# Performance work log

Measured on AMD Instinct MI355X. Metric: run time of the kernel, lower is better.

## Reference

```python
import jax, jax.numpy as jnp
import numpy as np

T, B, L, S = 2048, 64, 32, 256
NEG = -1e30  # effective -inf, safe under logaddexp


def setup_inputs() -> dict:
    key = jax.random.key(0)
    k1, k2, k3 = jax.random.split(key, 3)
    inputs = jax.random.normal(k1, (T, B, L), dtype=jnp.float32)
    targets = jax.random.randint(k2, (B, S), 0, L)
    input_lengths = jnp.full((B,), T, dtype=jnp.int32)
    target_lengths = jnp.full((B,), S, dtype=jnp.int32)
    # learned transition matrix (param of ASGLoss); small random for a non-trivial test
    transition = 0.1 * jax.random.normal(k3, (L, L), dtype=jnp.float32)
    return {"transition": transition, "inputs": inputs, "targets": targets,
            "input_lengths": input_lengths, "target_lengths": target_lengths}


def _fcc_scores(transition, inputs, input_lengths):
    # Fully-connected forward: alpha_t[i] = emit_t[i] + logsumexp_j(alpha_{t-1}[j] + trans[i,j])
    alpha0 = inputs[0]  # [B, L]

    def step(alpha, emit):
        new = emit + jax.nn.logsumexp(alpha[:, None, :] + transition[None, :, :], axis=2)
        return new, new

    _, rest = jax.lax.scan(step, alpha0, inputs[1:])
    alphas = jnp.concatenate([alpha0[None], rest], axis=0)  # [T, B, L]
    b = jnp.arange(inputs.shape[1])
    # causal DP: alpha at t = len-1 is exactly the score for that length
    return jax.nn.logsumexp(alphas[input_lengths - 1, b], axis=-1)  # [B]


def _fac_scores(transition, inputs, targets, input_lengths, target_lengths):
    # Force-aligned forward over target positions s:
    # alpha_t[s] = emit_t[tgt_s] + logaddexp(alpha_{t-1}[s] + trans[tgt_s,tgt_s],
    #                                        alpha_{t-1}[s-1] + trans[tgt_s,tgt_{s-1}])
    Tn, Bn, _ = inputs.shape
    Sn = targets.shape[1]
    # gathered emissions for target labels: [T, B, S]
    emit = jnp.take_along_axis(inputs, jnp.broadcast_to(targets[None], (Tn, Bn, Sn)), axis=2)
    self_tr = transition[targets, targets]                       # [B, S] stay score
    prev = jnp.concatenate([targets[:, :1], targets[:, :-1]], 1)
    move_tr = transition[targets, prev]                          # [B, S] move score (s=0 unused)

    alpha0 = jnp.where((jnp.arange(Sn) == 0)[None, :], emit[0], NEG)  # only s=0 at t=0

    def step(alpha, e):
        stay = alpha + self_tr
        moved = jnp.concatenate(
            [jnp.full_like(alpha[:, :1], NEG), alpha[:, :-1] + move_tr[:, 1:]], axis=1)
        new = e + jnp.logaddexp(stay, moved)
        return new, new

    _, rest = jax.lax.scan(step, alpha0, emit[1:])
    alphas = jnp.concatenate([alpha0[None], rest], axis=0)  # [T, B, S]
    b = jnp.arange(Bn)
    return alphas[input_lengths - 1, b, target_lengths - 1]  # [B]


def reference(transition, inputs, targets, input_lengths, target_lengths):
    # original clamps targets to input length; S <= T here so it's a no-op
    fcc = _fcc_scores(transition, inputs, input_lengths)
    fac = _fac_scores(transition, inputs, targets, input_lengths, target_lengths)
    result = fcc - fac  # [B]
    return result.mean()  # reduction='mean'
```

## Files before the change

### kernel.cpp

```cpp
#include <hip/hip_runtime.h>
#include <math.h>

static constexpr int TB = 64;
static constexpr int LL = 32;
static constexpr int SS = 256;
static constexpr int STRIDE_T = TB * LL;

static constexpr int NCH = 16;
static constexpr int NI  = NCH - 2;
static constexpr int NSCAN = 2 + 2 * NI;

static constexpr int OF_FCC  = 0;
static constexpr int OF_FACF = 992;
static constexpr int OF_FACB = 1312;
static constexpr int WSB     = 1632;
static constexpr int OF_DIFF = TB * WSB;

#define LN2F 0.69314718055994530942f
#define NEGF (-1e30f)
#define SBAR() __builtin_amdgcn_sched_barrier(0)

#define BARX() { asm volatile("s_waitcnt lgkmcnt(0)" ::: "memory"); \
                 __builtin_amdgcn_s_barrier(); \
                 asm volatile("" ::: "memory"); }

template<int CTL>
__device__ __forceinline__ float dpp_f(float x, float oldv) {
  return __int_as_float(__builtin_amdgcn_update_dpp(
      __float_as_int(oldv), __float_as_int(x), CTL, 0xF, 0xF, false));
}
template<int M>
__device__ __forceinline__ int rot_i(int x) {
  return __builtin_amdgcn_update_dpp(0, x, 0x120 + M, 0xF, 0xF, false);
}

typedef unsigned uint2v __attribute__((ext_vector_type(2)));
__device__ __forceinline__ float xsum16(float x) {
  uint2v r = __builtin_amdgcn_permlane16_swap(__float_as_uint(x), __float_as_uint(x), false, false);
  return __uint_as_float(r.x) + __uint_as_float(r.y);
}
__device__ __forceinline__ float xsum32(float x) {
  uint2v r = __builtin_amdgcn_permlane32_swap(__float_as_uint(x), __float_as_uint(x), false, false);
  return __uint_as_float(r.x) + __uint_as_float(r.y);
}
__device__ __forceinline__ float bperm(int addr, float src) {
  return __int_as_float(__builtin_amdgcn_ds_bpermute(addr, __float_as_int(src)));
}

template<int M>
struct Calib {
  __device__ static __forceinline__ void run(const float* trans, int lam, int i, float* Ec) {
    Ec[M] = __expf(trans[i * LL + rot_i<M>(lam)]);
    Calib<M + 1>::run(trans, lam, i, Ec);
  }
};
template<> struct Calib<16> {
  __device__ static __forceinline__ void run(const float*, int, int, float*) {}
};
template<int M>
struct CalibT {
  __device__ static __forceinline__ void run(const float* trans, int lam, int i, float* Ec) {
    Ec[M] = __expf(trans[rot_i<M>(lam) * LL + i]);
    CalibT<M + 1>::run(trans, lam, i, Ec);
  }
};
template<> struct CalibT<16> {
  __device__ static __forceinline__ void run(const float*, int, int, float*) {}
};

#define ROT_MUL(DST, SRC, COEF, ROT) \
  asm("v_mul_f32_dpp %0, %1, %2 row_ror:" #ROT " row_mask:0xf bank_mask:0xf" \
      : "=v"(DST) : "v"(SRC), "v"(COEF))
#define ROT_FMAC(ACC, SRC, COEF, ROT) \
  asm("v_fmac_f32_dpp %0, %1, %2 row_ror:" #ROT " row_mask:0xf bank_mask:0xf" \
      : "+v"(ACC) : "v"(SRC), "v"(COEF))

#define STEP16(EC) { \
  float a0 = EC[0] * A, a1, a2, a3, a4, a5, a6, a7; \
  ROT_MUL(a1, A, EC[1], 1); ROT_MUL(a2, A, EC[2], 2); ROT_MUL(a3, A, EC[3], 3); \
  ROT_MUL(a4, A, EC[4], 4); ROT_MUL(a5, A, EC[5], 5); ROT_MUL(a6, A, EC[6], 6); \
  ROT_MUL(a7, A, EC[7], 7); \
  ROT_FMAC(a0, A, EC[8], 8);   ROT_FMAC(a1, A, EC[9], 9); \
  ROT_FMAC(a2, A, EC[10], 10); ROT_FMAC(a3, A, EC[11], 11); \
  ROT_FMAC(a4, A, EC[12], 12); ROT_FMAC(a5, A, EC[13], 13); \
  ROT_FMAC(a6, A, EC[14], 14); ROT_FMAC(a7, A, EC[15], 15); \
  part = ((a0 + a1) + (a2 + a3)) + ((a4 + a5) + (a6 + a7)); }


#define FCC_RENORM() { \
  unsigned uu = (unsigned)__builtin_amdgcn_readfirstlane((int)__float_as_uint(A)); \
  int ex = (int)((uu >> 23) & 255) - 127; \
  A = ldexpf(A, -ex); Kt += ex; }

#define LDBLK(R, TBASE) { \
  _Pragma("unroll") for (int k = 0; k < 4; ++k) { \
    int tt = (TBASE) + 2 * k + rowoff; tt = tt > lenm1 ? lenm1 : tt; \
    R[k] = gpl[(size_t)tt * STRIDE_T]; } \
  SBAR(); }
#define LDBLKD(R, TBASE) { \
  _Pragma("unroll") for (int k = 0; k < 4; ++k) { \
    int tt = (TBASE) + 2 * k + rowoff; \
    tt = tt < 0 ? 0 : (tt > lenm1 ? lenm1 : tt); \
    R[k] = gpl[(size_t)tt * STRIDE_T]; } \
  SBAR(); }

#define FCC_BLOCK8(R) { \
  float eb[8]; \
  _Pragma("unroll") for (int k = 0; k < 4; ++k) { \
    float e_ = __expf(R[k]); \
    eb[2 * k]     = bperm(adE, e_); \
    eb[2 * k + 1] = bperm(adO, e_); } \
  { float part; STEP16(Ec1); A = eb[0] * xsum16(part); } \
  { float part; STEP16(Ec2); A = eb[1] * xsum32(part); } \
  { float part; STEP16(Ec1); A = eb[2] * xsum16(part); } \
  { float part; STEP16(Ec2); A = eb[3] * xsum32(part); } \
  { float part; STEP16(Ec1); A = eb[4] * xsum16(part); } \
  { float part; STEP16(Ec2); A = eb[5] * xsum32(part); } \
  { float part; STEP16(Ec1); A = eb[6] * xsum16(part); } \
  { float part; STEP16(Ec2); A = eb[7] * xsum32(part); } \
  FCC_RENORM(); }

#define FCC_BWDBLK8(R) { \
  float eb[8]; \
  _Pragma("unroll") for (int k = 0; k < 4; ++k) { \
    float e_ = __expf(R[k]); \
    eb[2 * k]     = bperm(adE, e_); \
    eb[2 * k + 1] = bperm(adO, e_); } \
  { A *= eb[7]; float part; STEP16(E1T); A = xsum16(part); } \
  { A *= eb[6]; float part; STEP16(E2T); A = xsum32(part); } \
  { A *= eb[5]; float part; STEP16(E1T); A = xsum16(part); } \
  { A *= eb[4]; float part; STEP16(E2T); A = xsum32(part); } \
  { A *= eb[3]; float part; STEP16(E1T); A = xsum16(part); } \
  { A *= eb[2]; float part; STEP16(E2T); A = xsum32(part); } \
  { A *= eb[1]; float part; STEP16(E1T); A = xsum16(part); } \
  { A *= eb[0]; float part; STEP16(E2T); A = xsum32(part); } \
  FCC_RENORM(); }


#define FAC_BOUNDARY_S() { \
  float maxA = fmaxf(fmaxf(A0, A1), fmaxf(A2, A3)); \
  if (maxA > 0.f) { \
    int ex = (int)((__float_as_uint(maxA) >> 23) & 255) - 127; \
    A0 = ldexpf(A0, -ex); A1 = ldexpf(A1, -ex); \
    A2 = ldexpf(A2, -ex); A3 = ldexpf(A3, -ex); \
    m += (float)ex; \
  } \
  float mp = dpp_f<0x138>(m, NEGF); m = (m == NEGF) ? mp : m; \
  mp = dpp_f<0x138>(m, NEGF);       m = (m == NEGF) ? mp : m; \
  mp = dpp_f<0x138>(m, NEGF); \
  float dlt = fminf(mp - m, 50.0f); \
  Sin = exp2f(dlt); }

#define FACB_BOUNDARY_S() { \
  float maxA = fmaxf(fmaxf(A0, A1), fmaxf(A2, A3)); \
  if (maxA > 0.f) { \
    int ex = (int)((__float_as_uint(maxA) >> 23) & 255) - 127; \
    A0 = ldexpf(A0, -ex); A1 = ldexpf(A1, -ex); \
    A2 = ldexpf(A2, -ex); A3 = ldexpf(A3, -ex); \
    m += (float)ex; \
  } \
  float mp = dpp_f<0x130>(m, NEGF); m = (m == NEGF) ? mp : m; \
  mp = dpp_f<0x130>(m, NEGF);       m = (m == NEGF) ? mp : m; \
  mp = dpp_f<0x130>(m, NEGF); \
  float dlt = fminf(mp - m, 50.0f); \
  Sb = exp2f(dlt); }

#define FRDGRP(PB, BASE) { \
  _Pragma("unroll") for (int r = 0; r < 8; ++r) { \
    e0[r] = sE[PB][(BASE) + r][tg[0]]; \
    e1[r] = sE[PB][(BASE) + r][tg[1]]; \
    e2[r] = sE[PB][(BASE) + r][tg[2]]; \
    e3[r] = sE[PB][(BASE) + r][tg[3]]; } \
  SBAR(); }

#define FSTEPN(R) { \
  float c0 = e0[R] * ST[0], c1 = e1[R] * ST[1]; \
  float c2 = e2[R] * ST[2], c3 = e3[R] * ST[3]; \
  float v0 = e0[R] * CM[0], v1 = e1[R] * CM[1]; \
  float v2 = e2[R] * CM[2], v3 = e3[R] * CM[3]; \
  float ap = dpp_f<0x138>(A3, 0.f);  \
  float n0 = fmaf(v0 * Sin, ap, c0 * A0); \
  float n1 = fmaf(v1, A0, c1 * A1); \
  float n2 = fmaf(v2, A1, c2 * A2); \
  float n3 = fmaf(v3, A2, c3 * A3); \
  A0 = n0; A1 = n1; A2 = n2; A3 = n3; }

#define FBSTEPN(R) { \
  float c0 = e0[R] * ST[0], c1 = e1[R] * ST[1]; \
  float c2 = e2[R] * ST[2], c3 = e3[R] * ST[3]; \
  float w0 = e1[R] * CM[0], w1 = e2[R] * CM[1], w2 = e3[R] * CM[2]; \
  float en3 = dpp_f<0x130>(e0[R], 0.f);  \
  float w3 = en3 * CM[3]; \
  float an = dpp_f<0x130>(A0, 0.f); \
  float n0 = fmaf(w0, A1, c0 * A0); \
  float n1 = fmaf(w1, A2, c1 * A1); \
  float n2 = fmaf(w2, A3, c2 * A2); \
  float n3 = fmaf(w3 * Sb, an, c3 * A3); \
  A0 = n0; A1 = n1; A2 = n2; A3 = n3; }

#define FACF_CON32N(PB) { \
  float e0[8], e1[8], e2[8], e3[8]; \
  FRDGRP(PB, 0); \
  _Pragma("unroll") for (int r = 0; r < 8; ++r) FSTEPN(r); \
  FAC_BOUNDARY_S(); \
  FRDGRP(PB, 8); \
  _Pragma("unroll") for (int r = 0; r < 8; ++r) FSTEPN(r); \
  FAC_BOUNDARY_S(); \
  FRDGRP(PB, 16); \
  _Pragma("unroll") for (int r = 0; r < 8; ++r) FSTEPN(r); \
  FAC_BOUNDARY_S(); \
  FRDGRP(PB, 24); \
  _Pragma("unroll") for (int r = 0; r < 8; ++r) FSTEPN(r); \
  FAC_BOUNDARY_S(); }

#define FACF_TAIL32N(PB, CNT) { \
  float e0[8], e1[8], e2[8], e3[8]; \
  _Pragma("unroll") for (int g4 = 0; g4 < 4; ++g4) { \
    if (8 * g4 >= (CNT)) break; \
    FRDGRP(PB, 8 * g4); \
    _Pragma("unroll") for (int r = 0; r < 8; ++r) { \
      if (8 * g4 + r >= (CNT)) break; \
      FSTEPN(r); } \
    if (8 * g4 + 8 <= (CNT)) { FAC_BOUNDARY_S(); } } }

#define FACB_CON32N(PB) { \
  float e0[8], e1[8], e2[8], e3[8]; \
  FRDGRP(PB, 24); \
  _Pragma("unroll") for (int i = 0; i < 8; ++i) { const int r = 7 - i; FBSTEPN(r); } \
  FACB_BOUNDARY_S(); \
  FRDGRP(PB, 16); \
  _Pragma("unroll") for (int i = 0; i < 8; ++i) { const int r = 7 - i; FBSTEPN(r); } \
  FACB_BOUNDARY_S(); \
  FRDGRP(PB, 8); \
  _Pragma("unroll") for (int i = 0; i < 8; ++i) { const int r = 7 - i; FBSTEPN(r); } \
  FACB_BOUNDARY_S(); \
  FRDGRP(PB, 0); \
  _Pragma("unroll") for (int i = 0; i < 8; ++i) { const int r = 7 - i; FBSTEPN(r); } \
  FACB_BOUNDARY_S(); }

#define PRODPH(PB, Q) { \
  _Pragma("unroll") for (int k = 0; k < 16; ++k) { \
    int tt = isfwd ? (1 + 32 * (Q) + 2 * k + rowoff) \
                   : (lenm1 - 32 * (Q) - 31 + 2 * k + rowoff); \
    tt = tt < 0 ? 0 : (tt > lenm1 ? lenm1 : tt); \
    float e_ = __expf(gpl[(size_t)tt * STRIDE_T]); \
    sE[PB][2 * k + rowoff][lam1] = e_; } \
  SBAR(); }


extern "C" __global__ __launch_bounds__(128, 1)
void asg_main(const float* __restrict__ trans, const float* __restrict__ inputs,
              const int* __restrict__ targets, const int* __restrict__ ilen,
              const int* __restrict__ tlen, float* __restrict__ ws) {
  const int tid = (int)threadIdx.x;
  const int w = tid >> 6;
  const int l = tid & 63;
  const int lam1 = l & 31;
  const int lam2 = (l & 15) | ((l >> 5) << 4);
  const int rowoff = l >> 5;
  const int bid = (int)blockIdx.x;

  __shared__ float sE[2][32][32];

  if (bid < 2 * TB) {
    const int role = bid >> 6;
    const int b    = bid & 63;
    const int len = ilen[b];
    const int lenm1 = len - 1;
    const int Lsteps = lenm1;
    const int nbf = (Lsteps / 2) & ~31;
    const int nff = Lsteps - nbf;
    const bool isfwd = (role == 0);
    const int nsteps = isfwd ? nff : nbf;
    const int nph = (nsteps + 31) >> 5;
    const float* gpl = inputs + (size_t)b * LL + lam1;
    float* P = ws + (size_t)b * WSB;

    if (w == 0) {
      __builtin_amdgcn_s_setprio(1);
      int tg[4];
      #pragma unroll
      for (int q = 0; q < 4; ++q) tg[q] = targets[b * SS + 4 * l + q];
      float ST[4], CM[4];
      #pragma unroll
      for (int q = 0; q < 4; ++q) ST[q] = __expf(trans[tg[q] * LL + tg[q]]);

      if (isfwd) {
        CM[0] = (l == 0) ? 0.f : __expf(trans[tg[0] * LL + targets[b * SS + 4 * l - 1]]);
        #pragma unroll
        for (int q = 1; q < 4; ++q) CM[q] = __expf(trans[tg[q] * LL + tg[q - 1]]);

        float A0 = (l == 0) ? __expf(inputs[(size_t)b * LL + tg[0]]) : 0.f;
        float A1 = 0.f, A2 = 0.f, A3 = 0.f;
        float m  = (l == 0) ? 0.f : NEGF;
        float Sin;
        FAC_BOUNDARY_S();
        for (int p = 0; p < nph; p += 2) {
          BARX();
          { const int rem = nsteps - 32 * p;
            if (rem >= 32) { FACF_CON32N(0); } else { FACF_TAIL32N(0, rem); } }
          BARX();
          if (p + 1 < nph) {
            const int rem = nsteps - 32 * (p + 1);
            if (rem >= 32) { FACF_CON32N(1); } else { FACF_TAIL32N(1, rem); }
          }
        }
        P[OF_FACF + 4 * l + 0] = A0;
        P[OF_FACF + 4 * l + 1] = A1;
        P[OF_FACF + 4 * l + 2] = A2;
        P[OF_FACF + 4 * l + 3] = A3;
        P[OF_FACF + 256 + l]   = m;
      } else {
        CM[0] = __expf(trans[tg[1] * LL + tg[0]]);
        CM[1] = __expf(trans[tg[2] * LL + tg[1]]);
        CM[2] = __expf(trans[tg[3] * LL + tg[2]]);
        int tgn3 = (l < 63) ? targets[b * SS + 4 * l + 4] : 0;
        CM[3] = (l < 63) ? __expf(trans[tgn3 * LL + tg[3]]) : 0.f;

        const int tl = tlen[b];
        const int fs = tl - 1;
        float A0 = (4 * l + 0 == fs) ? 1.f : 0.f;
        float A1 = (4 * l + 1 == fs) ? 1.f : 0.f;
        float A2 = (4 * l + 2 == fs) ? 1.f : 0.f;
        float A3 = (4 * l + 3 == fs) ? 1.f : 0.f;
        float m  = (l == (fs >> 2)) ? 0.f : NEGF;
        float Sb;
        FACB_BOUNDARY_S();
        for (int p = 0; p < nph; p += 2) {
          BARX();
          FACB_CON32N(0);
          BARX();
          if (p + 1 < nph) { FACB_CON32N(1); }
        }
        P[OF_FACB + 4 * l + 0] = A0;
        P[OF_FACB + 4 * l + 1] = A1;
        P[OF_FACB + 4 * l + 2] = A2;
        P[OF_FACB + 4 * l + 3] = A3;
        P[OF_FACB + 256 + l]   = m;
      }
    } else {
      PRODPH(0, 0);
      for (int p = 0; p < nph; p += 2) {
        BARX();
        if (p + 1 < nph) { PRODPH(1, p + 1); }
        BARX();
        if (p + 2 < nph) { PRODPH(0, p + 2); }
      }
    }
    return;
  }

  const int cid = bid - 2 * TB;
  const int sid = 2 * cid + w;
  const int s = sid >> 6;
  const int b = sid & 63;
  const int len = ilen[b];
  const int lenm1 = len - 1;
  const int Lsteps = lenm1;
  int L = ((Lsteps / NCH) + 4) & ~7;
  if ((NCH - 1) * L > Lsteps) L = (Lsteps / NCH) & ~7;
  const int n0 = Lsteps - (NCH - 1) * L;

  bool isfwd; int t0 = 1, thi = lenm1, nsteps, outslot;
  if (s == 0)      { isfwd = true;  t0 = 1; nsteps = n0; outslot = 0; }
  else if (s == 1) { isfwd = false; thi = lenm1; nsteps = L; outslot = 1; }
  else {
    const int j = s >> 1;
    if ((s & 1) == 0) { isfwd = true;  t0 = n0 + (j - 1) * L + 1; nsteps = L; outslot = 2 * j; }
    else              { isfwd = false; thi = n0 + j * L;          nsteps = L; outslot = 2 * j + 1; }
  }
  const float* gpl = inputs + (size_t)b * LL + lam1;
  float* P = ws + (size_t)b * WSB + OF_FCC + outslot * 33;

  const int adE = lam2 * 4;
  const int adO = 128 + lam1 * 4;

  if (isfwd) {
    float Ec1[16], Ec2[16];
    Ec1[0] = __expf(trans[lam2 * LL + lam1]);
    Ec2[0] = __expf(trans[lam1 * LL + lam2]);
    Calib<1>::run(trans, lam1, lam2, Ec1);
    Calib<1>::run(trans, lam2, lam1, Ec2);
    float A = (s == 0) ? __expf(inputs[(size_t)b * LL + lam1]) : 1.f;
    int Kt = 0;
    int t = t0;
    const int tend = t0 + nsteps;
    float R0_[4], R1_[4], R2_[4];
    LDBLK(R0_, t); LDBLK(R1_, t + 8); LDBLK(R2_, t + 16);
    for (;;) {
      if (t + 8 > tend) break;
      FCC_BLOCK8(R0_); LDBLK(R0_, t + 24); t += 8;
      if (t + 8 > tend) break;
      FCC_BLOCK8(R1_); LDBLK(R1_, t + 24); t += 8;
      if (t + 8 > tend) break;
      FCC_BLOCK8(R2_); LDBLK(R2_, t + 24); t += 8;
    }
    if (t < tend) {
      float RT[4];
      LDBLK(RT, t);
      float eb[8];
      #pragma unroll
      for (int k = 0; k < 4; ++k) {
        float e_ = __expf(RT[k]);
        eb[2 * k]     = bperm(adE, e_);
        eb[2 * k + 1] = bperm(adO, e_);
      }
      #pragma unroll
      for (int q = 0; q < 8; ++q) {
        if (t + q >= tend) break;
        if ((q & 1) == 0) { float part; STEP16(Ec1); A = eb[q] * xsum16(part); }
        else              { float part; STEP16(Ec2); A = eb[q] * xsum32(part); }
      }
    }
    const int par = nsteps & 1;
    const int idx = par ? lam2 : lam1;
    const bool wr = par ? ((l & 16) == 0) : (l < 32);
    if (wr) P[idx] = A;
    if (l == 0) P[32] = (float)Kt;

  } else {
    float E1T[16], E2T[16];
    E1T[0] = __expf(trans[lam1 * LL + lam2]);
    E2T[0] = __expf(trans[lam2 * LL + lam1]);
    CalibT<1>::run(trans, lam1, lam2, E1T);
    CalibT<1>::run(trans, lam2, lam1, E2T);
    float A = 1.f;
    int Kt = 0;
    int th = thi;
    int rem = nsteps;
    float R0_[4], R1_[4], R2_[4];
    LDBLKD(R0_, th - 7); LDBLKD(R1_, th - 15); LDBLKD(R2_, th - 23);
    for (;;) {
      if (rem < 8) break;
      FCC_BWDBLK8(R0_); LDBLKD(R0_, th - 31); th -= 8; rem -= 8;
      if (rem < 8) break;
      FCC_BWDBLK8(R1_); LDBLKD(R1_, th - 31); th -= 8; rem -= 8;
      if (rem < 8) break;
      FCC_BWDBLK8(R2_); LDBLKD(R2_, th - 31); th -= 8; rem -= 8;
    }
    if (l < 32) P[lam1] = A;
    if (l == 0) P[32] = (float)Kt;
  }
}


extern "C" __global__ __launch_bounds__(64)
void asg_combineA(const float* __restrict__ ws, float* __restrict__ wdiff) {
  const int b = (int)blockIdx.x;
  const int l = (int)threadIdx.x;
  const float* P = ws + (size_t)b * WSB;

  float acc = 0.f;
  float Ksum = P[OF_FCC + 0 * 33 + 32];
  #pragma unroll
  for (int j = 0; j <= NI; ++j) {
    const int qs = (j == NI) ? 1 : (2 * j + 3);
    const int ps = (j == 0) ? 0 : (2 * j);
    float qv = (l < 32) ? P[OF_FCC + qs * 33 + l] : 0.f;
    float pv = (l < 32) ? P[OF_FCC + ps * 33 + l] : 0.f;
    float d = qv * pv;
    #pragma unroll
    for (int mm = 1; mm < 64; mm <<= 1) d += __shfl_xor(d, mm);
    acc += __logf(d);
    Ksum += P[OF_FCC + qs * 33 + 32];
  }
  #pragma unroll
  for (int j = 1; j <= NI; ++j) {
    float pv = (l < 32) ? P[OF_FCC + 2 * j * 33 + l] : 0.f;
    #pragma unroll
    for (int mm = 1; mm < 64; mm <<= 1) pv += __shfl_xor(pv, mm);
    acc -= __logf(pv);
  }
  float fcc = acc + Ksum * LN2F;

  float pa = P[OF_FACF + 4 * l + 0] * P[OF_FACB + 4 * l + 0]
           + P[OF_FACF + 4 * l + 1] * P[OF_FACB + 4 * l + 1]
           + P[OF_FACF + 4 * l + 2] * P[OF_FACB + 4 * l + 2]
           + P[OF_FACF + 4 * l + 3] * P[OF_FACB + 4 * l + 3];
  float sc = P[OF_FACF + 256 + l] + P[OF_FACB + 256 + l];
  float Ms = sc;
  #pragma unroll
  for (int mm = 1; mm < 64; mm <<= 1) Ms = fmaxf(Ms, __shfl_xor(Ms, mm));
  float pp = pa * exp2f(sc - Ms);
  #pragma unroll
  for (int mm = 1; mm < 64; mm <<= 1) pp += __shfl_xor(pp, mm);
  float fac = __logf(pp) + Ms * LN2F;

  if (l == 0) wdiff[b] = fcc - fac;
}

extern "C" __global__ __launch_bounds__(64)
void asg_combineB(const float* __restrict__ wdiff, float* __restrict__ out) {
  const int l = (int)threadIdx.x;
  float d = wdiff[l];
  #pragma unroll
  for (int mm = 1; mm < 64; mm <<= 1) d += __shfl_xor(d, mm);
  if (l == 0) out[0] = d * (1.0f / TB);
}


extern "C" void kernel_launch(void* const* d_in, const int* in_sizes, int n_in,
                              void* d_out, int out_size, void* d_ws, size_t ws_size,
                              hipStream_t stream) {
  const float* trans   = (const float*)d_in[0];
  const float* inputs  = (const float*)d_in[1];
  const int*   targets = (const int*)d_in[2];
  const int*   ilen    = (const int*)d_in[3];
  const int*   tlen    = (const int*)d_in[4];
  float* out = (float*)d_out;
  float* ws  = (float*)d_ws;

  asg_main<<<dim3(2 * TB + (NSCAN * TB) / 2), dim3(128), 0, stream>>>(
      trans, inputs, targets, ilen, tlen, ws);
  asg_combineA<<<dim3(TB), dim3(64), 0, stream>>>(ws, ws + OF_DIFF);
  asg_combineB<<<dim3(1), dim3(64), 0, stream>>>(ws + OF_DIFF, out);
}
```

Baseline: 78.34 us.

## Merge producer into consumer wave and pack eight waves per block

The force-aligned DP waves no longer rely on a separate producer wave and block barriers. Each wave now loads its own emissions into registers, exponentiates them into a private LDS slice and software-pipelines the next phase's loads with the current phase's compute. Blocks grow to 512 threads holding eight independent waves, which shrinks the grid to 16 FAC blocks plus the scan blocks. This removes the barrier handoff, but the serial DP wave now also does the exp and store work, and any wave-to-wave ordering on its LDS slice rests only on lgkmcnt waits, which may be fragile.

```diff
diff --git a/kernel.cpp b/kernel.cpp
--- a/kernel.cpp
+++ b/kernel.cpp
@@ -19,10 +19,6 @@
 #define LN2F 0.69314718055994530942f
 #define NEGF (-1e30f)
 #define SBAR() __builtin_amdgcn_sched_barrier(0)
-
-#define BARX() { asm volatile("s_waitcnt lgkmcnt(0)" ::: "memory"); \
-                 __builtin_amdgcn_s_barrier(); \
-                 asm volatile("" ::: "memory"); }
 
 template<int CTL>
 __device__ __forceinline__ float dpp_f(float x, float oldv) {
@@ -137,6 +133,8 @@
   FCC_RENORM(); }
 
 
+#define MYE(PB, ROW, LBL) myE[(PB) * 1024 + (ROW) * 32 + (LBL)]
+
 #define FAC_BOUNDARY_S() { \
   float maxA = fmaxf(fmaxf(A0, A1), fmaxf(A2, A3)); \
   if (maxA > 0.f) { \
@@ -167,10 +165,10 @@
 
 #define FRDGRP(PB, BASE) { \
   _Pragma("unroll") for (int r = 0; r < 8; ++r) { \
-    e0[r] = sE[PB][(BASE) + r][tg[0]]; \
-    e1[r] = sE[PB][(BASE) + r][tg[1]]; \
-    e2[r] = sE[PB][(BASE) + r][tg[2]]; \
-    e3[r] = sE[PB][(BASE) + r][tg[3]]; } \
+    e0[r] = MYE(PB, (BASE) + r, tg[0]); \
+    e1[r] = MYE(PB, (BASE) + r, tg[1]); \
+    e2[r] = MYE(PB, (BASE) + r, tg[2]); \
+    e3[r] = MYE(PB, (BASE) + r, tg[3]); } \
   SBAR(); }
 
 #define FSTEPN(R) { \
@@ -238,17 +236,20 @@
   _Pragma("unroll") for (int i = 0; i < 8; ++i) { const int r = 7 - i; FBSTEPN(r); } \
   FACB_BOUNDARY_S(); }
 
-#define PRODPH(PB, Q) { \
+#define SLD(Q) { \
   _Pragma("unroll") for (int k = 0; k < 16; ++k) { \
     int tt = isfwd ? (1 + 32 * (Q) + 2 * k + rowoff) \
                    : (lenm1 - 32 * (Q) - 31 + 2 * k + rowoff); \
     tt = tt < 0 ? 0 : (tt > lenm1 ? lenm1 : tt); \
-    float e_ = __expf(gpl[(size_t)tt * STRIDE_T]); \
-    sE[PB][2 * k + rowoff][lam1] = e_; } \
+    R[k] = gpl[(size_t)tt * STRIDE_T]; } \
   SBAR(); }
-
-
-extern "C" __global__ __launch_bounds__(128, 1)
+#define SWR(PB) { \
+  _Pragma("unroll") for (int k = 0; k < 16; ++k) { \
+    MYE(PB, 2 * k + rowoff, lam1) = __expf(R[k]); } \
+  SBAR(); }
+
+
+extern "C" __global__ __launch_bounds__(512, 1)
 void asg_main(const float* __restrict__ trans, const float* __restrict__ inputs,
               const int* __restrict__ targets, const int* __restrict__ ilen,
               const int* __restrict__ tlen, float* __restrict__ ws) {
@@ -260,11 +261,12 @@
   const int rowoff = l >> 5;
   const int bid = (int)blockIdx.x;
 
-  __shared__ float sE[2][32][32];
-
-  if (bid < 2 * TB) {
-    const int role = bid >> 6;
-    const int b    = bid & 63;
+  __shared__ float sE[8][2048];
+
+  if (bid < 16) {
+    const int hid = bid * 8 + w;
+    const int role = hid >> 6;
+    const int b    = hid & 63;
     const int len = ilen[b];
     const int lenm1 = len - 1;
     const int Lsteps = lenm1;
@@ -275,83 +277,81 @@
     const int nph = (nsteps + 31) >> 5;
     const float* gpl = inputs + (size_t)b * LL + lam1;
     float* P = ws + (size_t)b * WSB;
-
-    if (w == 0) {
-      __builtin_amdgcn_s_setprio(1);
-      int tg[4];
+    float* myE = &sE[w][0];
+
+    int tg[4];
+    #pragma unroll
+    for (int q = 0; q < 4; ++q) tg[q] = targets[b * SS + 4 * l + q];
+    float ST[4], CM[4];
+    #pragma unroll
+    for (int q = 0; q < 4; ++q) ST[q] = __expf(trans[tg[q] * LL + tg[q]]);
+
+    float R[16];
+
+    if (isfwd) {
+      CM[0] = (l == 0) ? 0.f : __expf(trans[tg[0] * LL + targets[b * SS + 4 * l - 1]]);
       #pragma unroll
-      for (int q = 0; q < 4; ++q) tg[q] = targets[b * SS + 4 * l + q];
-      float ST[4], CM[4];
-      #pragma unroll
-      for (int q = 0; q < 4; ++q) ST[q] = __expf(trans[tg[q] * LL + tg[q]]);
-
-      if (isfwd) {
-        CM[0] = (l == 0) ? 0.f : __expf(trans[tg[0] * LL + targets[b * SS + 4 * l - 1]]);
-        #pragma unroll
-        for (int q = 1; q < 4; ++q) CM[q] = __expf(trans[tg[q] * LL + tg[q - 1]]);
-
-        float A0 = (l == 0) ? __expf(inputs[(size_t)b * LL + tg[0]]) : 0.f;
-        float A1 = 0.f, A2 = 0.f, A3 = 0.f;
-        float m  = (l == 0) ? 0.f : NEGF;
-        float Sin;
-        FAC_BOUNDARY_S();
-        for (int p = 0; p < nph; p += 2) {
-          BARX();
-          { const int rem = nsteps - 32 * p;
-            if (rem >= 32) { FACF_CON32N(0); } else { FACF_TAIL32N(0, rem); } }
-          BARX();
-          if (p + 1 < nph) {
-            const int rem = nsteps - 32 * (p + 1);
-            if (rem >= 32) { FACF_CON32N(1); } else { FACF_TAIL32N(1, rem); }
-          }
-        }
-        P[OF_FACF + 4 * l + 0] = A0;
-        P[OF_FACF + 4 * l + 1] = A1;
-        P[OF_FACF + 4 * l + 2] = A2;
-        P[OF_FACF + 4 * l + 3] = A3;
-        P[OF_FACF + 256 + l]   = m;
-      } else {
-        CM[0] = __expf(trans[tg[1] * LL + tg[0]]);
-        CM[1] = __expf(trans[tg[2] * LL + tg[1]]);
-        CM[2] = __expf(trans[tg[3] * LL + tg[2]]);
-        int tgn3 = (l < 63) ? targets[b * SS + 4 * l + 4] : 0;
-        CM[3] = (l < 63) ? __expf(trans[tgn3 * LL + tg[3]]) : 0.f;
-
-        const int tl = tlen[b];
-        const int fs = tl - 1;
-        float A0 = (4 * l + 0 == fs) ? 1.f : 0.f;
-        float A1 = (4 * l + 1 == fs) ? 1.f : 0.f;
-        float A2 = (4 * l + 2 == fs) ? 1.f : 0.f;
-        float A3 = (4 * l + 3 == fs) ? 1.f : 0.f;
-        float m  = (l == (fs >> 2)) ? 0.f : NEGF;
-        float Sb;
-        FACB_BOUNDARY_S();
-        for (int p = 0; p < nph; p += 2) {
-          BARX();
-          FACB_CON32N(0);
-          BARX();
-          if (p + 1 < nph) { FACB_CON32N(1); }
-        }
-        P[OF_FACB + 4 * l + 0] = A0;
-        P[OF_FACB + 4 * l + 1] = A1;
-        P[OF_FACB + 4 * l + 2] = A2;
-        P[OF_FACB + 4 * l + 3] = A3;
-        P[OF_FACB + 256 + l]   = m;
+      for (int q = 1; q < 4; ++q) CM[q] = __expf(trans[tg[q] * LL + tg[q - 1]]);
+
+      float A0 = (l == 0) ? __expf(inputs[(size_t)b * LL + tg[0]]) : 0.f;
+      float A1 = 0.f, A2 = 0.f, A3 = 0.f;
+      float m  = (l == 0) ? 0.f : NEGF;
+      float Sin;
+      FAC_BOUNDARY_S();
+
+      SLD(0); SWR(0);
+      if (nph > 1) { SLD(1); }
+      asm volatile("s_waitcnt lgkmcnt(0)" ::: "memory");
+      for (int p = 0; p < nph; ++p) {
+        if (p + 1 < nph) { SWR((p + 1) & 1); }
+        if (p + 2 < nph) { SLD(p + 2); }
+        const int rem = nsteps - 32 * p;
+        const int pb = p & 1;
+        if (rem >= 32) { FACF_CON32N(pb); } else { FACF_TAIL32N(pb, rem); }
       }
+      P[OF_FACF + 4 * l + 0] = A0;
+      P[OF_FACF + 4 * l + 1] = A1;
+      P[OF_FACF + 4 * l + 2] = A2;
+      P[OF_FACF + 4 * l + 3] = A3;
+      P[OF_FACF + 256 + l]   = m;
+
     } else {
-      PRODPH(0, 0);
-      for (int p = 0; p < nph; p += 2) {
-        BARX();
-        if (p + 1 < nph) { PRODPH(1, p + 1); }
-        BARX();
-        if (p + 2 < nph) { PRODPH(0, p + 2); }
+      CM[0] = __expf(trans[tg[1] * LL + tg[0]]);
+      CM[1] = __expf(trans[tg[2] * LL + tg[1]]);
+      CM[2] = __expf(trans[tg[3] * LL + tg[2]]);
+      int tgn3 = (l < 63) ? targets[b * SS + 4 * l + 4] : 0;
+      CM[3] = (l < 63) ? __expf(trans[tgn3 * LL + tg[3]]) : 0.f;
+
+      const int tl = tlen[b];
+      const int fs = tl - 1;
+      float A0 = (4 * l + 0 == fs) ? 1.f : 0.f;
+      float A1 = (4 * l + 1 == fs) ? 1.f : 0.f;
+      float A2 = (4 * l + 2 == fs) ? 1.f : 0.f;
+      float A3 = (4 * l + 3 == fs) ? 1.f : 0.f;
+      float m  = (l == (fs >> 2)) ? 0.f : NEGF;
+      float Sb;
+      FACB_BOUNDARY_S();
+
+      SLD(0); SWR(0);
+      if (nph > 1) { SLD(1); }
+      asm volatile("s_waitcnt lgkmcnt(0)" ::: "memory");
+      for (int p = 0; p < nph; ++p) {
+        if (p + 1 < nph) { SWR((p + 1) & 1); }
+        if (p + 2 < nph) { SLD(p + 2); }
+        const int pb = p & 1;
+        FACB_CON32N(pb);
       }
+      P[OF_FACB + 4 * l + 0] = A0;
+      P[OF_FACB + 4 * l + 1] = A1;
+      P[OF_FACB + 4 * l + 2] = A2;
+      P[OF_FACB + 4 * l + 3] = A3;
+      P[OF_FACB + 256 + l]   = m;
     }
     return;
   }
 
-  const int cid = bid - 2 * TB;
-  const int sid = 2 * cid + w;
+  const int cid = bid - 16;
+  const int sid = cid * 8 + w;
   const int s = sid >> 6;
   const int b = sid & 63;
   const int len = ilen[b];
@@ -510,7 +510,7 @@
   float* out = (float*)d_out;
   float* ws  = (float*)d_ws;
 
-  asg_main<<<dim3(2 * TB + (NSCAN * TB) / 2), dim3(128), 0, stream>>>(
+  asg_main<<<dim3(16 + (NSCAN * TB) / 8), dim3(512), 0, stream>>>(
       trans, inputs, targets, ilen, tlen, ws);
   asg_combineA<<<dim3(TB), dim3(64), 0, stream>>>(ws, ws + OF_DIFF);
   asg_combineB<<<dim3(1), dim3(64), 0, stream>>>(ws + OF_DIFF, out);
```

New measurement: 130.9 us. +67.1%, slower.

## Fuse combine kernels into main kernel via atomic last-arriver counters

Applied to the files above, without the earlier changes.

Removes the two follow-up combine kernel launches. Each contributing wave increments a per-batch atomic counter, and the last arriver performs the per-batch combine. A second global counter elects the final wave that computes the mean. A memset is added to zero the counters each launch. The forward/backward split for the force-aligned pass is also changed to round the backward share up to a multiple of 32, which rebalances the two chains.

```diff
diff --git a/kernel.cpp b/kernel.cpp
--- a/kernel.cpp
+++ b/kernel.cpp
@@ -9,12 +9,14 @@
 static constexpr int NCH = 16;
 static constexpr int NI  = NCH - 2;
 static constexpr int NSCAN = 2 + 2 * NI;
+static constexpr int NCONTRIB = NSCAN + 2;
 
 static constexpr int OF_FCC  = 0;
 static constexpr int OF_FACF = 992;
 static constexpr int OF_FACB = 1312;
 static constexpr int WSB     = 1632;
 static constexpr int OF_DIFF = TB * WSB;
+static constexpr int OF_CNT  = OF_DIFF + TB;
 
 #define LN2F 0.69314718055994530942f
 #define NEGF (-1e30f)
@@ -85,6 +87,72 @@
   ROT_FMAC(a4, A, EC[12], 12); ROT_FMAC(a5, A, EC[13], 13); \
   ROT_FMAC(a6, A, EC[14], 14); ROT_FMAC(a7, A, EC[15], 15); \
   part = ((a0 + a1) + (a2 + a3)) + ((a4 + a5) + (a6 + a7)); }
+
+
+__device__ __forceinline__ void finish_wave(float* __restrict__ ws,
+                                            float* __restrict__ out,
+                                            int b, int l) {
+  unsigned* cnt = (unsigned*)(ws + OF_CNT);
+  __threadfence();
+  int old = 0;
+  if (l == 0) old = (int)atomicAdd(&cnt[b], 1u);
+  old = __builtin_amdgcn_readfirstlane(old);
+  if (old != NCONTRIB - 1) return;
+
+  __threadfence();
+  const float* P = ws + (size_t)b * WSB;
+
+  float acc = 0.f;
+  float Ksum = P[OF_FCC + 0 * 33 + 32];
+  #pragma unroll
+  for (int j = 0; j <= NI; ++j) {
+    const int qs = (j == NI) ? 1 : (2 * j + 3);
+    const int ps = (j == 0) ? 0 : (2 * j);
+    float qv = (l < 32) ? P[OF_FCC + qs * 33 + l] : 0.f;
+    float pv = (l < 32) ? P[OF_FCC + ps * 33 + l] : 0.f;
+    float d = qv * pv;
+    #pragma unroll
+    for (int mm = 1; mm < 64; mm <<= 1) d += __shfl_xor(d, mm);
+    acc += __logf(d);
+    Ksum += P[OF_FCC + qs * 33 + 32];
+  }
+  #pragma unroll
+  for (int j = 1; j <= NI; ++j) {
+    float pv = (l < 32) ? P[OF_FCC + 2 * j * 33 + l] : 0.f;
+    #pragma unroll
+    for (int mm = 1; mm < 64; mm <<= 1) pv += __shfl_xor(pv, mm);
+    acc -= __logf(pv);
+  }
+  float fcc = acc + Ksum * LN2F;
+
+  float pa = P[OF_FACF + 4 * l + 0] * P[OF_FACB + 4 * l + 0]
+           + P[OF_FACF + 4 * l + 1] * P[OF_FACB + 4 * l + 1]
+           + P[OF_FACF + 4 * l + 2] * P[OF_FACB + 4 * l + 2]
+           + P[OF_FACF + 4 * l + 3] * P[OF_FACB + 4 * l + 3];
+  float sc = P[OF_FACF + 256 + l] + P[OF_FACB + 256 + l];
+  float Ms = sc;
+  #pragma unroll
+  for (int mm = 1; mm < 64; mm <<= 1) Ms = fmaxf(Ms, __shfl_xor(Ms, mm));
+  float pp = pa * exp2f(sc - Ms);
+  #pragma unroll
+  for (int mm = 1; mm < 64; mm <<= 1) pp += __shfl_xor(pp, mm);
+  float fac = __logf(pp) + Ms * LN2F;
+
+  float* wdiff = ws + OF_DIFF;
+  if (l == 0) wdiff[b] = fcc - fac;
+
+  __threadfence();
+  int o2 = 0;
+  if (l == 0) o2 = (int)atomicAdd(&cnt[TB], 1u);
+  o2 = __builtin_amdgcn_readfirstlane(o2);
+  if (o2 != TB - 1) return;
+
+  __threadfence();
+  float d = wdiff[l];
+  #pragma unroll
+  for (int mm = 1; mm < 64; mm <<= 1) d += __shfl_xor(d, mm);
+  if (l == 0) out[0] = d * (1.0f / TB);
+}
 
 
 #define FCC_RENORM() { \
@@ -251,7 +319,8 @@
 extern "C" __global__ __launch_bounds__(128, 1)
 void asg_main(const float* __restrict__ trans, const float* __restrict__ inputs,
               const int* __restrict__ targets, const int* __restrict__ ilen,
-              const int* __restrict__ tlen, float* __restrict__ ws) {
+              const int* __restrict__ tlen, float* __restrict__ ws,
+              float* __restrict__ out) {
   const int tid = (int)threadIdx.x;
   const int w = tid >> 6;
   const int l = tid & 63;
@@ -268,7 +337,8 @@
     const int len = ilen[b];
     const int lenm1 = len - 1;
     const int Lsteps = lenm1;
-    const int nbf = (Lsteps / 2) & ~31;
+    int nbf = ((Lsteps / 2) + 31) & ~31;
+    if (nbf > Lsteps) nbf = (Lsteps / 2) & ~31;
     const int nff = Lsteps - nbf;
     const bool isfwd = (role == 0);
     const int nsteps = isfwd ? nff : nbf;
@@ -338,6 +408,7 @@
         P[OF_FACB + 4 * l + 3] = A3;
         P[OF_FACB + 256 + l]   = m;
       }
+      finish_wave(ws, out, b, l);
     } else {
       PRODPH(0, 0);
       for (int p = 0; p < nph; p += 2) {
@@ -441,61 +512,7 @@
     if (l < 32) P[lam1] = A;
     if (l == 0) P[32] = (float)Kt;
   }
-}
-
-
-extern "C" __global__ __launch_bounds__(64)
-void asg_combineA(const float* __restrict__ ws, float* __restrict__ wdiff) {
-  const int b = (int)blockIdx.x;
-  const int l = (int)threadIdx.x;
-  const float* P = ws + (size_t)b * WSB;
-
-  float acc = 0.f;
-  float Ksum = P[OF_FCC + 0 * 33 + 32];
-  #pragma unroll
-  for (int j = 0; j <= NI; ++j) {
-    const int qs = (j == NI) ? 1 : (2 * j + 3);
-    const int ps = (j == 0) ? 0 : (2 * j);
-    float qv = (l < 32) ? P[OF_FCC + qs * 33 + l] : 0.f;
-    float pv = (l < 32) ? P[OF_FCC + ps * 33 + l] : 0.f;
-    float d = qv * pv;
-    #pragma unroll
-    for (int mm = 1; mm < 64; mm <<= 1) d += __shfl_xor(d, mm);
-    acc += __logf(d);
-    Ksum += P[OF_FCC + qs * 33 + 32];
-  }
-  #pragma unroll
-  for (int j = 1; j <= NI; ++j) {
-    float pv = (l < 32) ? P[OF_FCC + 2 * j * 33 + l] : 0.f;
-    #pragma unroll
-    for (int mm = 1; mm < 64; mm <<= 1) pv += __shfl_xor(pv, mm);
-    acc -= __logf(pv);
-  }
-  float fcc = acc + Ksum * LN2F;
-
-  float pa = P[OF_FACF + 4 * l + 0] * P[OF_FACB + 4 * l + 0]
-           + P[OF_FACF + 4 * l + 1] * P[OF_FACB + 4 * l + 1]
-           + P[OF_FACF + 4 * l + 2] * P[OF_FACB + 4 * l + 2]
-           + P[OF_FACF + 4 * l + 3] * P[OF_FACB + 4 * l + 3];
-  float sc = P[OF_FACF + 256 + l] + P[OF_FACB + 256 + l];
-  float Ms = sc;
-  #pragma unroll
-  for (int mm = 1; mm < 64; mm <<= 1) Ms = fmaxf(Ms, __shfl_xor(Ms, mm));
-  float pp = pa * exp2f(sc - Ms);
-  #pragma unroll
-  for (int mm = 1; mm < 64; mm <<= 1) pp += __shfl_xor(pp, mm);
-  float fac = __logf(pp) + Ms * LN2F;
-
-  if (l == 0) wdiff[b] = fcc - fac;
-}
-
-extern "C" __global__ __launch_bounds__(64)
-void asg_combineB(const float* __restrict__ wdiff, float* __restrict__ out) {
-  const int l = (int)threadIdx.x;
-  float d = wdiff[l];
-  #pragma unroll
-  for (int mm = 1; mm < 64; mm <<= 1) d += __shfl_xor(d, mm);
-  if (l == 0) out[0] = d * (1.0f / TB);
+  finish_wave(ws, out, b, l);
 }
 
 
@@ -510,8 +527,7 @@
   float* out = (float*)d_out;
   float* ws  = (float*)d_ws;
 
+  hipMemsetAsync(ws + OF_CNT, 0, (TB + 1) * sizeof(unsigned), stream);
   asg_main<<<dim3(2 * TB + (NSCAN * TB) / 2), dim3(128), 0, stream>>>(
-      trans, inputs, targets, ilen, tlen, ws);
-  asg_combineA<<<dim3(TB), dim3(64), 0, stream>>>(ws, ws + OF_DIFF);
-  asg_combineB<<<dim3(1), dim3(64), 0, stream>>>(ws + OF_DIFF, out);
-}
+      trans, inputs, targets, ilen, tlen, ws, out);
+}
```

Measured after the change: 112.7 us. +43.8%, slower.
